# Kernel tuning notes

Hardware: AMD Instinct MI355X
Metric: run time of the kernel (lower is better)

## Reference

```python
import jax, jax.numpy as jnp
import numpy as np

ALPHA = 0.01  # LeakyReLU negative slope
D_OUT = 128   # output_size; a1 is split at this index


def setup_inputs() -> dict:
    key = jax.random.key(0)
    k1, k2, k3, k4 = jax.random.split(key, 4)
    B, N, M, D_IN = 8, 2048, 2048, 256
    input_tensor1 = jax.random.normal(k1, (B, N, D_IN), dtype=jnp.float32)
    input_tensor2 = jax.random.normal(k2, (B, M, D_IN), dtype=jnp.float32)
    attention_mask2 = jnp.zeros((B, 1, M), dtype=jnp.float32)
    # Parameters (xavier-uniform-like scaled normals are fine for a numeric reference)
    W1 = jax.random.normal(k3, (D_IN, D_OUT), dtype=jnp.float32) * (1.414 * np.sqrt(2.0 / (D_IN + D_OUT)))
    a1 = jax.random.normal(k4, (2 * D_OUT, 1), dtype=jnp.float32) * (1.414 * np.sqrt(2.0 / (2 * D_OUT + 1)))
    return {"input_tensor1": input_tensor1, "input_tensor2": input_tensor2,
            "attention_mask2": attention_mask2, "W1": W1, "a1": a1}


def reference(input_tensor1, input_tensor2, attention_mask2, W1, a1):
    # Projections (dropout is identity in eval / p=0)
    Wh1 = jnp.einsum('bnd,de->bne', input_tensor1, W1)  # (B, N, E)
    Wh2 = jnp.einsum('bmd,de->bme', input_tensor2, W1)  # (B, M, E)
    # GAT-style additive score: broadcast outer-sum of two rank-1 projections
    att1 = jnp.einsum('bne,eo->bno', Wh1, a1[:D_OUT, :])   # (B, N, 1)
    att2 = jnp.einsum('bme,eo->bmo', Wh2, a1[D_OUT:, :])   # (B, M, 1)
    e = att1 + jnp.swapaxes(att2, 1, 2)                     # (B, N, M)
    e = jnp.where(e > 0, e, ALPHA * e)                      # LeakyReLU
    scores = e + attention_mask2                            # additive mask
    probs = jax.nn.softmax(scores, axis=-1)                 # (B, N, M)
    context = jnp.einsum('bnm,bme->bne', probs, Wh2)        # (B, N, E)
    return (context, probs)
```

## Files before the change

### kernel.cpp

```cpp
#include <hip/hip_runtime.h>

#define B 8
#define N 2048
#define M 2048
#define DIN 256
#define E 128
#define ALPHA 0.01f

typedef __attribute__((ext_vector_type(8))) short bf16x8;
typedef __attribute__((ext_vector_type(4))) float f32x4;

__device__ inline ushort f2bf(float x) {
  unsigned u = __float_as_uint(x);
  u = (u + 0x7FFFu + ((u >> 16) & 1u)) >> 16;
  return (ushort)u;
}

__global__ __launch_bounds__(256) void prep_v_kernel(
    const float* __restrict__ W1, const float* __restrict__ a1,
    float* __restrict__ v1, float* __restrict__ v2) {
  int k = threadIdx.x;
  float s1 = 0.f, s2 = 0.f;
#pragma unroll 8
  for (int e = 0; e < E; ++e) {
    float w = W1[k * E + e];
    s1 += w * a1[e];
    s2 += w * a1[E + e];
  }
  v1[k] = s1;
  v2[k] = s2;
}

__global__ __launch_bounds__(256) void att_kernel(
    const float* __restrict__ in1, const float* __restrict__ in2,
    const float* __restrict__ v1, const float* __restrict__ v2,
    float* __restrict__ att1, float* __restrict__ att2) {
  int wave = blockIdx.x * 4 + (threadIdx.x >> 6);
  int lane = threadIdx.x & 63;
  const float* src;
  const float* v;
  float* dst;
  int row;
  if (wave < B * N) {
    src = in1; v = v1; dst = att1; row = wave;
  } else {
    src = in2; v = v2; dst = att2; row = wave - B * N;
  }
  float4 x = *(const float4*)(src + (size_t)row * DIN + lane * 4);
  float4 vv = *(const float4*)(v + lane * 4);
  float d = x.x * vv.x + x.y * vv.y + x.z * vv.z + x.w * vv.w;
#pragma unroll
  for (int off = 32; off; off >>= 1) d += __shfl_down(d, off, 64);
  if (lane == 0) dst[row] = d;
}

__global__ __launch_bounds__(256) void wh2_kernel(
    const float* __restrict__ in2, const float* __restrict__ W1,
    ushort* __restrict__ Wb) {
  __shared__ float a[32][DIN];
  int r0 = blockIdx.x * 32;
#pragma unroll
  for (int i = 0; i < 8; ++i) {
    int f = (threadIdx.x + i * 256) * 4;
    int r = f >> 8, k = f & 255;
    *(float4*)&a[r][k] = *(const float4*)(in2 + (size_t)(r0 + r) * DIN + k);
  }
  __syncthreads();
  int c  = (threadIdx.x & 31) * 4;
  int tr = (threadIdx.x >> 5) * 4;
  float acc[4][4] = {};
  for (int k = 0; k < DIN; ++k) {
    float4 b = *(const float4*)(W1 + k * E + c);
#pragma unroll
    for (int r = 0; r < 4; ++r) {
      float av = a[tr + r][k];
      acc[r][0] += av * b.x;
      acc[r][1] += av * b.y;
      acc[r][2] += av * b.z;
      acc[r][3] += av * b.w;
    }
  }
#pragma unroll
  for (int r = 0; r < 4; ++r) {
    int m = r0 + tr + r;
    size_t gbase = (size_t)(m >> 3) * 128 * 8 + (m & 7);
#pragma unroll
    for (int j = 0; j < 4; ++j)
      Wb[gbase + (size_t)(c + j) * 8] = f2bf(acc[r][j]);
  }
}

__global__ __launch_bounds__(256) void fused_kernel(
    const float* __restrict__ att1, const float* __restrict__ att2,
    const float* __restrict__ mask, const ushort* __restrict__ Wb,
    float* __restrict__ probs, float* __restrict__ ctx) {
  __shared__ float att2s[M];
  __shared__ float masks[M];
  __shared__ float att1s[32];
  __shared__ float red[32][9];
  __shared__ float rowmax[32];
  __shared__ float rowinv[32];
  __shared__ ushort ldsB[8 * 128 * 8];

  int rt = blockIdx.x & 63;
  int b  = blockIdx.x >> 6;
  int row0 = b * N + rt * 32;
  int t = threadIdx.x;

#pragma unroll
  for (int i = 0; i < 2; ++i) {
    int idx = (t + i * 256) * 4;
    *(float4*)&att2s[idx] = *(const float4*)(att2 + b * M + idx);
    *(float4*)&masks[idx] = *(const float4*)(mask + b * M + idx);
  }
  if (t < 32) att1s[t] = att1[row0 + t];
  __syncthreads();

  int r = t >> 3, ch = t & 7;
  float a1r = att1s[r];
  float mx = -1e30f;
  for (int m = ch * 256; m < ch * 256 + 256; ++m) {
    float s = a1r + att2s[m];
    s = s > 0.f ? s : ALPHA * s;
    s += masks[m];
    mx = fmaxf(mx, s);
  }
  red[r][ch] = mx;
  __syncthreads();
  if (t < 32) {
    float m2 = red[t][0];
#pragma unroll
    for (int j = 1; j < 8; ++j) m2 = fmaxf(m2, red[t][j]);
    rowmax[t] = m2;
  }
  __syncthreads();
  float rmax = rowmax[r];
  float sum = 0.f;
  for (int m = ch * 256; m < ch * 256 + 256; ++m) {
    float s = a1r + att2s[m];
    s = s > 0.f ? s : ALPHA * s;
    s += masks[m];
    sum += __expf(s - rmax);
  }
  red[r][ch] = sum;
  __syncthreads();
  if (t < 32) {
    float s2 = 0.f;
#pragma unroll
    for (int j = 0; j < 8; ++j) s2 += red[t][j];
    rowinv[t] = 1.f / s2;
  }
  __syncthreads();

  int lane = t & 63;
  int w = t >> 6;
  int quad = lane >> 4;
  int l16 = lane & 15;
  int m0w = (w & 1) * 16;
  int n0w = (w >> 1) * 64;
  float a1v  = att1s[m0w + l16];
  float rmxL = rowmax[m0w + l16];
  float rinL = rowinv[m0w + l16];
  bool do_store = (n0w == 0);
  float* prow = probs + (size_t)(row0 + m0w + l16) * M;

  f32x4 acc[4] = {};

  for (int k0 = 0; k0 < M; k0 += 64) {
    {
      const char* g =
          (const char*)(Wb + (size_t)(b * 256 + (k0 >> 3)) * 128 * 8);
      char* l = (char*)ldsB;
      int base = w * 4096 + lane * 16;
#pragma unroll
      for (int i = 0; i < 4; ++i) {
        int off = base + i * 1024;
        __builtin_amdgcn_global_load_lds(
            (const __attribute__((address_space(1))) void*)(g + off),
            (__attribute__((address_space(3))) void*)(l + off), 16, 0, 0);
      }
    }
    __syncthreads();
#pragma unroll
    for (int ks = 0; ks < 64; ks += 32) {
      int kb = k0 + ks + quad * 8;
      bf16x8 af;
      float p[8];
#pragma unroll
      for (int j = 0; j < 8; ++j) {
        float s = a1v + att2s[kb + j];
        s = s > 0.f ? s : ALPHA * s;
        s += masks[kb + j];
        float pe = __expf(s - rmxL) * rinL;
        p[j] = pe;
        af[j] = (short)f2bf(pe);
      }
      if (do_store) {
        *(float4*)(prow + kb)     = make_float4(p[0], p[1], p[2], p[3]);
        *(float4*)(prow + kb + 4) = make_float4(p[4], p[5], p[6], p[7]);
      }
      int gl = (ks >> 3) + quad;
#pragma unroll
      for (int cf = 0; cf < 4; ++cf) {
        int n = n0w + cf * 16 + l16;
        bf16x8 bfb = *(const bf16x8*)&ldsB[((size_t)gl * 128 + n) * 8];
        acc[cf] =
            __builtin_amdgcn_mfma_f32_16x16x32_bf16(af, bfb, acc[cf], 0, 0, 0);
      }
    }
    __syncthreads();
  }
#pragma unroll
  for (int cf = 0; cf < 4; ++cf) {
    int nn = n0w + cf * 16 + l16;
#pragma unroll
    for (int reg = 0; reg < 4; ++reg) {
      int rr = row0 + m0w + quad * 4 + reg;
      ctx[(size_t)rr * E + nn] = acc[cf][reg];
    }
  }
}

extern "C" void kernel_launch(void* const* d_in, const int* in_sizes, int n_in,
                              void* d_out, int out_size, void* d_ws,
                              size_t ws_size, hipStream_t stream) {
  (void)in_sizes; (void)n_in; (void)out_size; (void)ws_size;
  const float* in1  = (const float*)d_in[0];
  const float* in2  = (const float*)d_in[1];
  const float* mask = (const float*)d_in[2];
  const float* W1   = (const float*)d_in[3];
  const float* a1   = (const float*)d_in[4];

  float* ws   = (float*)d_ws;
  float* v1   = ws;
  float* v2   = v1 + DIN;
  float* att1 = v2 + DIN;
  float* att2 = att1 + B * N;
  ushort* Wb  = (ushort*)(att2 + B * M);

  float* ctx   = (float*)d_out;
  float* probs = ctx + (size_t)B * N * E;

  hipLaunchKernelGGL(prep_v_kernel, dim3(1), dim3(256), 0, stream, W1, a1, v1, v2);
  hipLaunchKernelGGL(att_kernel, dim3((B * N + B * M) / 4), dim3(256), 0, stream,
                     in1, in2, v1, v2, att1, att2);
  hipLaunchKernelGGL(wh2_kernel, dim3(B * M / 32), dim3(256), 0, stream,
                     in2, W1, Wb);
  hipLaunchKernelGGL(fused_kernel, dim3(B * N / 32), dim3(256), 0, stream,
                     att1, att2, mask, Wb, probs, ctx);
}
```

Before: 266.7 us.

## Move softmax stats to separate kernel and split K across waves in fused kernel

Row max and sum-of-exp are now computed in a separate stats kernel, one wave per row, and stored to workspace, so the fused kernel no longer runs two serial passes over 2048 columns with block reductions. In the fused kernel, the two wave pairs now split the K range instead of the output columns. Each wave computes its own probabilities, with no duplicated exp work and all waves storing probs, then the partial accumulators are summed through LDS at the end. This adds a kernel launch, some workspace traffic, and more accumulator registers per wave.

```diff
diff --git a/kernel.cpp b/kernel.cpp
--- a/kernel.cpp
+++ b/kernel.cpp
@@ -14,6 +14,12 @@
   unsigned u = __float_as_uint(x);
   u = (u + 0x7FFFu + ((u >> 16) & 1u)) >> 16;
   return (ushort)u;
+}
+
+__device__ inline float leaky_mask(float a1r, float a2, float mk) {
+  float s = a1r + a2;
+  s = s > 0.f ? s : ALPHA * s;
+  return s + mk;
 }
 
 __global__ __launch_bounds__(256) void prep_v_kernel(
@@ -90,119 +96,124 @@
   }
 }
 
+__global__ __launch_bounds__(256) void stats_kernel(
+    const float* __restrict__ att1, const float* __restrict__ att2,
+    const float* __restrict__ mask,
+    float* __restrict__ rowmax, float* __restrict__ rowinv) {
+  int row = blockIdx.x * 4 + (threadIdx.x >> 6);
+  int lane = threadIdx.x & 63;
+  int b = row >> 11;
+  float a1r = att1[row];
+  const float* a2 = att2 + b * M;
+  const float* mk = mask + b * M;
+  float mx = -1e30f;
+#pragma unroll
+  for (int i = 0; i < 8; ++i) {
+    int m = (lane + i * 64) * 4;
+    float4 av = *(const float4*)(a2 + m);
+    float4 mv = *(const float4*)(mk + m);
+    mx = fmaxf(mx, leaky_mask(a1r, av.x, mv.x));
+    mx = fmaxf(mx, leaky_mask(a1r, av.y, mv.y));
+    mx = fmaxf(mx, leaky_mask(a1r, av.z, mv.z));
+    mx = fmaxf(mx, leaky_mask(a1r, av.w, mv.w));
+  }
+#pragma unroll
+  for (int off = 32; off; off >>= 1) mx = fmaxf(mx, __shfl_xor(mx, off, 64));
+  float sum = 0.f;
+#pragma unroll
+  for (int i = 0; i < 8; ++i) {
+    int m = (lane + i * 64) * 4;
+    float4 av = *(const float4*)(a2 + m);
+    float4 mv = *(const float4*)(mk + m);
+    sum += __expf(leaky_mask(a1r, av.x, mv.x) - mx);
+    sum += __expf(leaky_mask(a1r, av.y, mv.y) - mx);
+    sum += __expf(leaky_mask(a1r, av.z, mv.z) - mx);
+    sum += __expf(leaky_mask(a1r, av.w, mv.w) - mx);
+  }
+#pragma unroll
+  for (int off = 32; off; off >>= 1) sum += __shfl_xor(sum, off, 64);
+  if (lane == 0) {
+    rowmax[row] = mx;
+    rowinv[row] = 1.f / sum;
+  }
+}
+
 __global__ __launch_bounds__(256) void fused_kernel(
     const float* __restrict__ att1, const float* __restrict__ att2,
-    const float* __restrict__ mask, const ushort* __restrict__ Wb,
+    const float* __restrict__ mask, const float* __restrict__ rowmax,
+    const float* __restrict__ rowinv, const ushort* __restrict__ Wb,
     float* __restrict__ probs, float* __restrict__ ctx) {
   __shared__ float att2s[M];
   __shared__ float masks[M];
-  __shared__ float att1s[32];
-  __shared__ float red[32][9];
-  __shared__ float rowmax[32];
-  __shared__ float rowinv[32];
-  __shared__ ushort ldsB[8 * 128 * 8];
+  __shared__ ushort ldsB[2 * 8 * 128 * 8];
 
   int rt = blockIdx.x & 63;
   int b  = blockIdx.x >> 6;
   int row0 = b * N + rt * 32;
   int t = threadIdx.x;
-
-#pragma unroll
-  for (int i = 0; i < 2; ++i) {
-    int idx = (t + i * 256) * 4;
-    *(float4*)&att2s[idx] = *(const float4*)(att2 + b * M + idx);
-    *(float4*)&masks[idx] = *(const float4*)(mask + b * M + idx);
-  }
-  if (t < 32) att1s[t] = att1[row0 + t];
-  __syncthreads();
-
-  int r = t >> 3, ch = t & 7;
-  float a1r = att1s[r];
-  float mx = -1e30f;
-  for (int m = ch * 256; m < ch * 256 + 256; ++m) {
-    float s = a1r + att2s[m];
-    s = s > 0.f ? s : ALPHA * s;
-    s += masks[m];
-    mx = fmaxf(mx, s);
-  }
-  red[r][ch] = mx;
-  __syncthreads();
-  if (t < 32) {
-    float m2 = red[t][0];
-#pragma unroll
-    for (int j = 1; j < 8; ++j) m2 = fmaxf(m2, red[t][j]);
-    rowmax[t] = m2;
-  }
-  __syncthreads();
-  float rmax = rowmax[r];
-  float sum = 0.f;
-  for (int m = ch * 256; m < ch * 256 + 256; ++m) {
-    float s = a1r + att2s[m];
-    s = s > 0.f ? s : ALPHA * s;
-    s += masks[m];
-    sum += __expf(s - rmax);
-  }
-  red[r][ch] = sum;
-  __syncthreads();
-  if (t < 32) {
-    float s2 = 0.f;
-#pragma unroll
-    for (int j = 0; j < 8; ++j) s2 += red[t][j];
-    rowinv[t] = 1.f / s2;
-  }
-  __syncthreads();
-
   int lane = t & 63;
   int w = t >> 6;
   int quad = lane >> 4;
   int l16 = lane & 15;
   int m0w = (w & 1) * 16;
-  int n0w = (w >> 1) * 64;
-  float a1v  = att1s[m0w + l16];
-  float rmxL = rowmax[m0w + l16];
-  float rinL = rowinv[m0w + l16];
-  bool do_store = (n0w == 0);
-  float* prow = probs + (size_t)(row0 + m0w + l16) * M;
-
-  f32x4 acc[4] = {};
-
-  for (int k0 = 0; k0 < M; k0 += 64) {
+  int h   = w >> 1;
+
+#pragma unroll
+  for (int i = 0; i < 2; ++i) {
+    int idx = (t + i * 256) * 4;
+    *(float4*)&att2s[idx] = *(const float4*)(att2 + b * M + idx);
+    *(float4*)&masks[idx] = *(const float4*)(mask + b * M + idx);
+  }
+
+  int myrow = row0 + m0w + l16;
+  float a1v  = att1[myrow];
+  float rmxL = rowmax[myrow];
+  float rinL = rowinv[myrow];
+  float* prow = probs + (size_t)myrow * M;
+
+  f32x4 acc[8] = {};
+
+  for (int k0 = 0; k0 < M; k0 += 128) {
     {
       const char* g =
-          (const char*)(Wb + (size_t)(b * 256 + (k0 >> 3)) * 128 * 8);
+          (const char*)(Wb + ((size_t)b * 256 + (k0 >> 3)) * 1024);
       char* l = (char*)ldsB;
-      int base = w * 4096 + lane * 16;
-#pragma unroll
-      for (int i = 0; i < 4; ++i) {
-        int off = base + i * 1024;
+      int base = w * 1024 + lane * 16;
+#pragma unroll
+      for (int i = 0; i < 8; ++i) {
+        int off = base + i * 4096;
         __builtin_amdgcn_global_load_lds(
             (const __attribute__((address_space(1))) void*)(g + off),
             (__attribute__((address_space(3))) void*)(l + off), 16, 0, 0);
       }
     }
     __syncthreads();
+    int kc = k0 + h * 64;
 #pragma unroll
     for (int ks = 0; ks < 64; ks += 32) {
-      int kb = k0 + ks + quad * 8;
+      int kb = kc + ks + quad * 8;
+      float4 a0 = *(const float4*)&att2s[kb];
+      float4 a1q = *(const float4*)&att2s[kb + 4];
+      float4 k0v = *(const float4*)&masks[kb];
+      float4 k1v = *(const float4*)&masks[kb + 4];
+      float p[8];
+      p[0] = __expf(leaky_mask(a1v, a0.x, k0v.x) - rmxL) * rinL;
+      p[1] = __expf(leaky_mask(a1v, a0.y, k0v.y) - rmxL) * rinL;
+      p[2] = __expf(leaky_mask(a1v, a0.z, k0v.z) - rmxL) * rinL;
+      p[3] = __expf(leaky_mask(a1v, a0.w, k0v.w) - rmxL) * rinL;
+      p[4] = __expf(leaky_mask(a1v, a1q.x, k1v.x) - rmxL) * rinL;
+      p[5] = __expf(leaky_mask(a1v, a1q.y, k1v.y) - rmxL) * rinL;
+      p[6] = __expf(leaky_mask(a1v, a1q.z, k1v.z) - rmxL) * rinL;
+      p[7] = __expf(leaky_mask(a1v, a1q.w, k1v.w) - rmxL) * rinL;
       bf16x8 af;
-      float p[8];
-#pragma unroll
-      for (int j = 0; j < 8; ++j) {
-        float s = a1v + att2s[kb + j];
-        s = s > 0.f ? s : ALPHA * s;
-        s += masks[kb + j];
-        float pe = __expf(s - rmxL) * rinL;
-        p[j] = pe;
-        af[j] = (short)f2bf(pe);
-      }
-      if (do_store) {
-        *(float4*)(prow + kb)     = make_float4(p[0], p[1], p[2], p[3]);
-        *(float4*)(prow + kb + 4) = make_float4(p[4], p[5], p[6], p[7]);
-      }
-      int gl = (ks >> 3) + quad;
-#pragma unroll
-      for (int cf = 0; cf < 4; ++cf) {
-        int n = n0w + cf * 16 + l16;
+#pragma unroll
+      for (int j = 0; j < 8; ++j) af[j] = (short)f2bf(p[j]);
+      *(float4*)(prow + kb)     = make_float4(p[0], p[1], p[2], p[3]);
+      *(float4*)(prow + kb + 4) = make_float4(p[4], p[5], p[6], p[7]);
+      int gl = h * 8 + (ks >> 3) + quad;
+#pragma unroll
+      for (int cf = 0; cf < 8; ++cf) {
+        int n = cf * 16 + l16;
         bf16x8 bfb = *(const bf16x8*)&ldsB[((size_t)gl * 128 + n) * 8];
         acc[cf] =
             __builtin_amdgcn_mfma_f32_16x16x32_bf16(af, bfb, acc[cf], 0, 0, 0);
@@ -210,13 +221,26 @@
     }
     __syncthreads();
   }
-#pragma unroll
-  for (int cf = 0; cf < 4; ++cf) {
-    int nn = n0w + cf * 16 + l16;
-#pragma unroll
-    for (int reg = 0; reg < 4; ++reg) {
-      int rr = row0 + m0w + quad * 4 + reg;
-      ctx[(size_t)rr * E + nn] = acc[cf][reg];
+
+  float* red = (float*)ldsB;
+  if (h == 1) {
+    int base = ((w & 1) * 64 + lane) * 36;
+#pragma unroll
+    for (int cf = 0; cf < 8; ++cf)
+      *(f32x4*)&red[base + cf * 4] = acc[cf];
+  }
+  __syncthreads();
+  if (h == 0) {
+    int base = ((w & 1) * 64 + lane) * 36;
+#pragma unroll
+    for (int cf = 0; cf < 8; ++cf) {
+      f32x4 o = *(const f32x4*)&red[base + cf * 4];
+      int nn = cf * 16 + l16;
+#pragma unroll
+      for (int reg = 0; reg < 4; ++reg) {
+        int rr = row0 + m0w + quad * 4 + reg;
+        ctx[(size_t)rr * E + nn] = acc[cf][reg] + o[reg];
+      }
     }
   }
 }
@@ -231,12 +255,14 @@
   const float* W1   = (const float*)d_in[3];
   const float* a1   = (const float*)d_in[4];
 
-  float* ws   = (float*)d_ws;
-  float* v1   = ws;
-  float* v2   = v1 + DIN;
-  float* att1 = v2 + DIN;
-  float* att2 = att1 + B * N;
-  ushort* Wb  = (ushort*)(att2 + B * M);
+  float* ws     = (float*)d_ws;
+  float* v1     = ws;
+  float* v2     = v1 + DIN;
+  float* att1   = v2 + DIN;
+  float* att2   = att1 + B * N;
+  float* rowmax = att2 + B * M;
+  float* rowinv = rowmax + B * N;
+  ushort* Wb    = (ushort*)(rowinv + B * N);
 
   float* ctx   = (float*)d_out;
   float* probs = ctx + (size_t)B * N * E;
@@ -246,6 +272,8 @@
                      in1, in2, v1, v2, att1, att2);
   hipLaunchKernelGGL(wh2_kernel, dim3(B * M / 32), dim3(256), 0, stream,
                      in2, W1, Wb);
+  hipLaunchKernelGGL(stats_kernel, dim3(B * N / 4), dim3(256), 0, stream,
+                     att1, att2, mask, rowmax, rowinv);
   hipLaunchKernelGGL(fused_kernel, dim3(B * N / 32), dim3(256), 0, stream,
-                     att1, att2, mask, Wb, probs, ctx);
-}
+                     att1, att2, mask, rowmax, rowinv, Wb, probs, ctx);
+}
```

Result: faster. 228.5 us (-14.3%).
